# Performance work log

Measured on AMD Instinct MI355X. Metric: run time of the kernel, lower is better.

The kernel has to match this reference:

```python
import jax, jax.numpy as jnp
import numpy as np


def setup_inputs() -> dict:
    key = jax.random.key(0)
    k1, k2 = jax.random.split(key)
    # Activations from two consecutive VGG conv blocks (pre-nonlinearity values).
    prev_x = jax.random.normal(k1, (128, 256, 28, 28), dtype=jnp.float32)
    curr_x = jax.random.normal(k2, (128, 512, 14, 14), dtype=jnp.float32)
    return {"prev_x": prev_x, "curr_x": curr_x}


def reference(prev_x, curr_x):
    # Binary activation masks, as in the torch code's (x > 0).detach().float().
    prev_act = (prev_x > 0).astype(prev_x.dtype)  # [B, Cp, Hp, Wp]
    curr_act = (curr_x > 0).astype(curr_x.dtype)  # [B, Cc, Hc, Wc]
    # Original quadruple loop: for each (s, c, x, y):
    #   correlations[s, :, :, :] += prev_act[s] * curr_act[s, c, x, y]
    # which collapses to prev_act[s] * curr_act[s].sum(); then sum over samples.
    curr_sum = curr_act.sum(axis=(1, 2, 3))                     # [B]
    correlations_total = jnp.einsum('bchw,b->chw', prev_act, curr_sum)  # [Cp, Hp, Wp]
    return correlations_total
```

## Files before the change

### kernel.cpp

```cpp
#include <hip/hip_runtime.h>


constexpr int NB       = 128;
constexpr int PREV_CHW = 256 * 28 * 28;
constexpr int CURR_CHW = 512 * 14 * 14;
constexpr int PREV_V2  = PREV_CHW / 2;
constexpr int CURR_V4  = CURR_CHW / 4;
constexpr int QUARTER  = CURR_V4 / 4;

__global__ void __launch_bounds__(256)
count_pos_kernel(const float* __restrict__ curr, float* __restrict__ partial) {
    const int b = blockIdx.x;
    const int q = blockIdx.y;
    const float4* p = reinterpret_cast<const float4*>(curr)
                      + (size_t)b * CURR_V4 + (size_t)q * QUARTER;
    int cnt = 0;
    for (int i = threadIdx.x; i < QUARTER; i += 256) {
        float4 v = p[i];
        cnt += (v.x > 0.0f);
        cnt += (v.y > 0.0f);
        cnt += (v.z > 0.0f);
        cnt += (v.w > 0.0f);
    }
    #pragma unroll
    for (int off = 32; off > 0; off >>= 1)
        cnt += __shfl_down(cnt, off, 64);
    __shared__ int wsum[4];
    if ((threadIdx.x & 63) == 0)
        wsum[threadIdx.x >> 6] = cnt;
    __syncthreads();
    if (threadIdx.x == 0)
        partial[q * NB + b] = (float)(wsum[0] + wsum[1] + wsum[2] + wsum[3]);
}

__global__ void __launch_bounds__(128)
corr_kernel(const float* __restrict__ prev, const float* __restrict__ partial,
            float* __restrict__ out) {
    __shared__ float s_sum[NB];
    const int t = threadIdx.x;
    s_sum[t] = partial[t] + partial[NB + t] + partial[2 * NB + t] + partial[3 * NB + t];
    __syncthreads();

    const int u = blockIdx.x * 128 + t;
    const float2* pv = reinterpret_cast<const float2*>(prev) + u;

    float2 acc = make_float2(0.0f, 0.0f);
    #pragma unroll 16
    for (int b = 0; b < NB; ++b) {
        const float2 v = pv[(size_t)b * PREV_V2];
        const float s = s_sum[b];
        acc.x += (v.x > 0.0f) ? s : 0.0f;
        acc.y += (v.y > 0.0f) ? s : 0.0f;
    }
    reinterpret_cast<float2*>(out)[u] = acc;
}

extern "C" void kernel_launch(void* const* d_in, const int* in_sizes, int n_in,
                              void* d_out, int out_size, void* d_ws, size_t ws_size,
                              hipStream_t stream) {
    const float* prev = (const float*)d_in[0];
    const float* curr = (const float*)d_in[1];
    float* out     = (float*)d_out;
    float* partial = (float*)d_ws;

    count_pos_kernel<<<dim3(NB, 4), 256, 0, stream>>>(curr, partial);
    corr_kernel<<<PREV_V2 / 128, 128, 0, stream>>>(prev, partial, out);
}
```

Before: 31.28 us.

## Fuse count and correlation into one cooperative kernel with bitmask prefetch

New measurement: 112.5 us. 260% more time.

```diff
diff --git a/kernel.cpp b/kernel.cpp
--- a/kernel.cpp
+++ b/kernel.cpp
@@ -1,33 +1,116 @@
 #include <hip/hip_runtime.h>
+#include <hip/hip_cooperative_groups.h>
+
+namespace cg = cooperative_groups;
 
 
 constexpr int NB       = 128;
+constexpr int CURR_CHW = 512 * 14 * 14;
 constexpr int PREV_CHW = 256 * 28 * 28;
-constexpr int CURR_CHW = 512 * 14 * 14;
-constexpr int PREV_V2  = PREV_CHW / 2;
-constexpr int CURR_V4  = CURR_CHW / 4;
-constexpr int QUARTER  = CURR_V4 / 4;
+constexpr int NBLK     = 512;
+constexpr int SLICE_V4 = CURR_CHW * NB / NBLK / 4;
+constexpr int COLS0    = NBLK * 256;
+constexpr int TWO_BLKS = (PREV_CHW - COLS0) / 256;
+
+__global__ void __launch_bounds__(256)
+fused_kernel(const float* __restrict__ prev, const float* __restrict__ curr,
+             float* __restrict__ out, unsigned int* __restrict__ slots) {
+    const int g = blockIdx.x;
+    const int t = threadIdx.x;
+
+    {
+        const float4* p4 = reinterpret_cast<const float4*>(curr) + (size_t)g * SLICE_V4;
+        unsigned int c = 0;
+        for (int i = t; i < SLICE_V4; i += 256) {
+            const float4 v = p4[i];
+            c += (v.x > 0.f) + (v.y > 0.f) + (v.z > 0.f) + (v.w > 0.f);
+        }
+        #pragma unroll
+        for (int off = 32; off > 0; off >>= 1)
+            c += __shfl_down(c, off, 64);
+        __shared__ unsigned int wred[4];
+        if ((t & 63) == 0) wred[t >> 6] = c;
+        __syncthreads();
+        if (t == 0)
+            __hip_atomic_store(&slots[g], wred[0] + wred[1] + wred[2] + wred[3],
+                               __ATOMIC_RELAXED, __HIP_MEMORY_SCOPE_AGENT);
+    }
+
+    const int col0 = g * 256 + t;
+    const bool two = (g < TWO_BLKS);
+    unsigned int m0[4], m1[4];
+    {
+        const float* b0p = prev + col0;
+        #pragma unroll
+        for (int w = 0; w < 4; ++w) {
+            unsigned int a = 0;
+            #pragma unroll 16
+            for (int bb = 0; bb < 32; ++bb)
+                a |= (b0p[(size_t)(w * 32 + bb) * PREV_CHW] > 0.f ? 1u : 0u) << bb;
+            m0[w] = a;
+        }
+        if (two) {
+            const float* b1p = prev + col0 + COLS0;
+            #pragma unroll
+            for (int w = 0; w < 4; ++w) {
+                unsigned int a = 0;
+                #pragma unroll 16
+                for (int bb = 0; bb < 32; ++bb)
+                    a |= (b1p[(size_t)(w * 32 + bb) * PREV_CHW] > 0.f ? 1u : 0u) << bb;
+                m1[w] = a;
+            }
+        } else {
+            m1[0] = m1[1] = m1[2] = m1[3] = 0u;
+        }
+    }
+
+    cg::this_grid().sync();
+
+    __shared__ float s_sum[NB];
+    if (t < NB) {
+        unsigned int s = 0;
+        #pragma unroll
+        for (int q = 0; q < 4; ++q)
+            s += __hip_atomic_load(&slots[4 * t + q],
+                                   __ATOMIC_RELAXED, __HIP_MEMORY_SCOPE_AGENT);
+        s_sum[t] = (float)s;
+    }
+    __syncthreads();
+
+    float o0 = 0.f, o1 = 0.f;
+    #pragma unroll
+    for (int w = 0; w < 4; ++w) {
+        const unsigned int a0 = m0[w], a1 = m1[w];
+        #pragma unroll
+        for (int bb = 0; bb < 32; ++bb) {
+            const float s = s_sum[w * 32 + bb];
+            o0 += ((a0 >> bb) & 1u) ? s : 0.f;
+            o1 += ((a1 >> bb) & 1u) ? s : 0.f;
+        }
+    }
+    out[col0] = o0;
+    if (two) out[col0 + COLS0] = o1;
+}
+
+constexpr int CURR_V4 = CURR_CHW / 4;
+constexpr int QUARTER = CURR_V4 / 4;
+constexpr int PREV_V2 = PREV_CHW / 2;
 
 __global__ void __launch_bounds__(256)
 count_pos_kernel(const float* __restrict__ curr, float* __restrict__ partial) {
-    const int b = blockIdx.x;
-    const int q = blockIdx.y;
+    const int b = blockIdx.x, q = blockIdx.y;
     const float4* p = reinterpret_cast<const float4*>(curr)
                       + (size_t)b * CURR_V4 + (size_t)q * QUARTER;
     int cnt = 0;
     for (int i = threadIdx.x; i < QUARTER; i += 256) {
-        float4 v = p[i];
-        cnt += (v.x > 0.0f);
-        cnt += (v.y > 0.0f);
-        cnt += (v.z > 0.0f);
-        cnt += (v.w > 0.0f);
+        const float4 v = p[i];
+        cnt += (v.x > 0.f) + (v.y > 0.f) + (v.z > 0.f) + (v.w > 0.f);
     }
     #pragma unroll
     for (int off = 32; off > 0; off >>= 1)
         cnt += __shfl_down(cnt, off, 64);
     __shared__ int wsum[4];
-    if ((threadIdx.x & 63) == 0)
-        wsum[threadIdx.x >> 6] = cnt;
+    if ((threadIdx.x & 63) == 0) wsum[threadIdx.x >> 6] = cnt;
     __syncthreads();
     if (threadIdx.x == 0)
         partial[q * NB + b] = (float)(wsum[0] + wsum[1] + wsum[2] + wsum[3]);
@@ -40,17 +123,15 @@
     const int t = threadIdx.x;
     s_sum[t] = partial[t] + partial[NB + t] + partial[2 * NB + t] + partial[3 * NB + t];
     __syncthreads();
-
     const int u = blockIdx.x * 128 + t;
     const float2* pv = reinterpret_cast<const float2*>(prev) + u;
-
-    float2 acc = make_float2(0.0f, 0.0f);
+    float2 acc = make_float2(0.f, 0.f);
     #pragma unroll 16
     for (int b = 0; b < NB; ++b) {
         const float2 v = pv[(size_t)b * PREV_V2];
         const float s = s_sum[b];
-        acc.x += (v.x > 0.0f) ? s : 0.0f;
-        acc.y += (v.y > 0.0f) ? s : 0.0f;
+        acc.x += (v.x > 0.f) ? s : 0.f;
+        acc.y += (v.y > 0.f) ? s : 0.f;
     }
     reinterpret_cast<float2*>(out)[u] = acc;
 }
@@ -60,9 +141,16 @@
                               hipStream_t stream) {
     const float* prev = (const float*)d_in[0];
     const float* curr = (const float*)d_in[1];
-    float* out     = (float*)d_out;
-    float* partial = (float*)d_ws;
+    float* out = (float*)d_out;
 
-    count_pos_kernel<<<dim3(NB, 4), 256, 0, stream>>>(curr, partial);
-    corr_kernel<<<PREV_V2 / 128, 128, 0, stream>>>(prev, partial, out);
+    unsigned int* slots = (unsigned int*)d_ws;
+    void* args[] = { (void*)&prev, (void*)&curr, (void*)&out, (void*)&slots };
+    hipError_t err = hipLaunchCooperativeKernel((const void*)fused_kernel,
+                                                dim3(NBLK), dim3(256),
+                                                args, 0, stream);
+    if (err != hipSuccess) {
+        float* partial = (float*)d_ws;
+        count_pos_kernel<<<dim3(NB, 4), 256, 0, stream>>>(curr, partial);
+        corr_kernel<<<PREV_V2 / 128, 128, 0, stream>>>(prev, partial, out);
+    }
 }
```
